# Optimization experiments

Measured on AMD Instinct MI355X. Metric: run time of the kernel, lower is better.

The kernel has to match this reference:

```python
import jax, jax.numpy as jnp
import numpy as np

NUM_CLASSES = 21


def setup_inputs() -> dict:
    key = jax.random.key(0)
    k1, k2 = jax.random.split(key)
    B, C, H, W = 8, NUM_CLASSES, 512, 512
    inputs = jax.random.normal(k1, (B, C, H, W), dtype=jnp.float32)
    targets = jax.random.randint(k2, (B, H, W), 0, C, dtype=jnp.int64)
    return {"inputs": inputs, "targets": targets}


def reference(inputs, targets):
    # inputs: [B, C, H, W] logits; targets: [B, H, W] int labels
    B, C, H, W = inputs.shape
    # Hard predictions are detached in the original (Variable(inputs.data...))
    predicts = jax.lax.stop_gradient(jnp.argmax(inputs, axis=1))  # [B, H, W]
    probs = jax.nn.softmax(inputs, axis=1)                        # [B, C, H, W]

    classes = jnp.arange(C)
    # Per-class binary masks, vectorized over C.
    # Note: the original's i==0 branch (invert nonzero/zero) reduces to the
    # same (x == i) indicator as the i>0 branch.
    pm = predicts[:, None, :, :] == classes[None, :, None, None]  # [B, C, H, W] bool
    tm = targets[:, None, :, :] == classes[None, :, None, None]   # [B, C, H, W] bool
    union_mask = (pm | tm).astype(probs.dtype)      # union with 2 -> 1 clamp
    intersect_mask = (pm & tm).astype(probs.dtype)

    # Soft-weighted per-class sums over batch-flattened spatial dims.
    union = jnp.sum(probs * union_mask, axis=(2, 3))        # [B, C]
    intersect = jnp.sum(probs * intersect_mask, axis=(2, 3))  # [B, C]

    ratio = intersect / jnp.maximum(union, 1.0)  # [B, C]
    # Per class: MSELoss(ratio, 1) = mean over batch; then sum over classes.
    iou_loss = jnp.sum(jnp.mean((ratio - 1.0) ** 2, axis=0))
    return iou_loss
```

## Files before the change

### kernel.cpp

```cpp
#include <hip/hip_runtime.h>

#define NCLS 21
#define HW (512 * 512)
#define BATCH 8
#define GRIDX 128
#define BLOCK 256
#define QUADS_PER_BLOCK ((HW / 4) / GRIDX)
#define ITERS (QUADS_PER_BLOCK / BLOCK)

#define WS_FLOATS (2 * BATCH * NCLS)

__global__ void zero_ws_kernel(float* ws) {
    int i = blockIdx.x * blockDim.x + threadIdx.x;
    if (i < WS_FLOATS) ws[i] = 0.0f;
}

__global__ __launch_bounds__(BLOCK) void iou_partial_kernel(
        const float* __restrict__ in,
        const int* __restrict__ tgt,
        float* __restrict__ ws) {
    const int b = blockIdx.y;
    const float4* __restrict__ in4 = (const float4*)(in + (size_t)b * NCLS * HW);
    const int4*   __restrict__ tb4 = (const int4*)(tgt + (size_t)b * HW);

    float u_acc[NCLS];
    float i_acc[NCLS];
    #pragma unroll
    for (int c = 0; c < NCLS; ++c) { u_acc[c] = 0.0f; i_acc[c] = 0.0f; }

    const int qbase = blockIdx.x * QUADS_PER_BLOCK;

    for (int it = 0; it < ITERS; ++it) {
        const int q = qbase + it * BLOCK + threadIdx.x;
        const int4 tq = tb4[q];
        const int t[4] = {tq.x, tq.y, tq.z, tq.w};

        float m[4], s[4], vt[4];
        int   am[4];

        {
            const float4 x = in4[q];
            const float v[4] = {x.x, x.y, x.z, x.w};
            #pragma unroll
            for (int j = 0; j < 4; ++j) {
                m[j] = v[j]; s[j] = 1.0f; am[j] = 0; vt[j] = v[j];
            }
        }
        #pragma unroll
        for (int c = 1; c < NCLS; ++c) {
            const float4 x = in4[(size_t)c * (HW / 4) + q];
            const float v[4] = {x.x, x.y, x.z, x.w};
            #pragma unroll
            for (int j = 0; j < 4; ++j) {
                const float mn = fmaxf(m[j], v[j]);
                s[j] = s[j] * __expf(m[j] - mn) + __expf(v[j] - mn);
                am[j] = (v[j] > m[j]) ? c : am[j];
                m[j] = mn;
                vt[j] = (c == t[j]) ? v[j] : vt[j];
            }
        }

        #pragma unroll
        for (int j = 0; j < 4; ++j) {
            const float inv    = 1.0f / s[j];
            const float p_pred = inv;
            const float p_t    = __expf(vt[j] - m[j]) * inv;
            const int   tj = t[j], aj = am[j];
            const float w_t = (tj == aj) ? 0.0f : p_t;
            const float ip  = (tj == aj) ? p_pred : 0.0f;
            #pragma unroll
            for (int c = 0; c < NCLS; ++c) {
                u_acc[c] += ((c == aj) ? p_pred : 0.0f) + ((c == tj) ? w_t : 0.0f);
                i_acc[c] += (c == aj) ? ip : 0.0f;
            }
        }
    }

    #pragma unroll
    for (int c = 0; c < NCLS; ++c) {
        #pragma unroll
        for (int off = 32; off > 0; off >>= 1) {
            u_acc[c] += __shfl_down(u_acc[c], off, 64);
            i_acc[c] += __shfl_down(i_acc[c], off, 64);
        }
    }

    __shared__ float s_u[NCLS];
    __shared__ float s_i[NCLS];
    if (threadIdx.x < NCLS) { s_u[threadIdx.x] = 0.0f; s_i[threadIdx.x] = 0.0f; }
    __syncthreads();
    if ((threadIdx.x & 63) == 0) {
        #pragma unroll
        for (int c = 0; c < NCLS; ++c) {
            atomicAdd(&s_u[c], u_acc[c]);
            atomicAdd(&s_i[c], i_acc[c]);
        }
    }
    __syncthreads();
    if (threadIdx.x < NCLS) {
        atomicAdd(&ws[b * NCLS + threadIdx.x], s_u[threadIdx.x]);
        atomicAdd(&ws[BATCH * NCLS + b * NCLS + threadIdx.x], s_i[threadIdx.x]);
    }
}

__global__ __launch_bounds__(BLOCK) void finalize_kernel(
        const float* __restrict__ ws, float* __restrict__ out) {
    __shared__ float red[BLOCK];
    const int i = threadIdx.x;
    float val = 0.0f;
    if (i < BATCH * NCLS) {
        const float u  = ws[i];
        const float it = ws[BATCH * NCLS + i];
        const float ratio = it / fmaxf(u, 1.0f);
        const float d = ratio - 1.0f;
        val = d * d;
    }
    red[i] = val;
    __syncthreads();
    for (int off = BLOCK / 2; off > 0; off >>= 1) {
        if (i < off) red[i] += red[i + off];
        __syncthreads();
    }
    if (i == 0) out[0] = red[0] / (float)BATCH;
}

extern "C" void kernel_launch(void* const* d_in, const int* in_sizes, int n_in,
                              void* d_out, int out_size, void* d_ws, size_t ws_size,
                              hipStream_t stream) {
    const float* in  = (const float*)d_in[0];
    const int*   tgt = (const int*)d_in[1];
    float* ws  = (float*)d_ws;
    float* out = (float*)d_out;

    zero_ws_kernel<<<1, 512, 0, stream>>>(ws);
    dim3 grid(GRIDX, BATCH);
    iou_partial_kernel<<<grid, BLOCK, 0, stream>>>(in, tgt, ws);
    finalize_kernel<<<1, BLOCK, 0, stream>>>(ws, out);
}
```

Measured before the change: 256.5 us.

## Issue all class loads up front, one quad per thread, two-pass softmax

Each thread now handles exactly one quad of pixels. It issues all 21 class float4 loads at once before any compute, which replaces the strided per-block loop and doubles the grid to cover the image. The online softmax is replaced by a max/argmax pass followed by a separate exp-sum pass, which removes the rescaling exp per class. The aim is more memory-level parallelism and fewer exp calls. In exchange, register pressure is high (84 floats of inputs plus 42 accumulators), and the cross-block reduction and atomics now happen twice as often per pixel.

Measured after the change: 256.9 us. No clear change (+0.2%).

```diff
diff --git a/kernel.cpp b/kernel.cpp
--- a/kernel.cpp
+++ b/kernel.cpp
@@ -2,11 +2,10 @@
 
 #define NCLS 21
 #define HW (512 * 512)
+#define NQ (HW / 4)
 #define BATCH 8
-#define GRIDX 128
+#define GRIDX 256
 #define BLOCK 256
-#define QUADS_PER_BLOCK ((HW / 4) / GRIDX)
-#define ITERS (QUADS_PER_BLOCK / BLOCK)
 
 #define WS_FLOATS (2 * BATCH * NCLS)
 
@@ -23,56 +22,53 @@
     const float4* __restrict__ in4 = (const float4*)(in + (size_t)b * NCLS * HW);
     const int4*   __restrict__ tb4 = (const int4*)(tgt + (size_t)b * HW);
 
+    const int q = blockIdx.x * BLOCK + threadIdx.x;
+
+    const int4 tq = tb4[q];
+    float4 x[NCLS];
+    #pragma unroll
+    for (int c = 0; c < NCLS; ++c)
+        x[c] = in4[(size_t)c * NQ + q];
+
+    const int t[4] = {tq.x, tq.y, tq.z, tq.w};
+    float vj[4][NCLS];
+    #pragma unroll
+    for (int c = 0; c < NCLS; ++c) {
+        vj[0][c] = x[c].x; vj[1][c] = x[c].y; vj[2][c] = x[c].z; vj[3][c] = x[c].w;
+    }
+
     float u_acc[NCLS];
     float i_acc[NCLS];
     #pragma unroll
     for (int c = 0; c < NCLS; ++c) { u_acc[c] = 0.0f; i_acc[c] = 0.0f; }
 
-    const int qbase = blockIdx.x * QUADS_PER_BLOCK;
-
-    for (int it = 0; it < ITERS; ++it) {
-        const int q = qbase + it * BLOCK + threadIdx.x;
-        const int4 tq = tb4[q];
-        const int t[4] = {tq.x, tq.y, tq.z, tq.w};
-
-        float m[4], s[4], vt[4];
-        int   am[4];
-
-        {
-            const float4 x = in4[q];
-            const float v[4] = {x.x, x.y, x.z, x.w};
-            #pragma unroll
-            for (int j = 0; j < 4; ++j) {
-                m[j] = v[j]; s[j] = 1.0f; am[j] = 0; vt[j] = v[j];
-            }
-        }
+    #pragma unroll
+    for (int j = 0; j < 4; ++j) {
+        float m = vj[j][0];
+        int   aj = 0;
+        float vt = vj[j][0];
         #pragma unroll
         for (int c = 1; c < NCLS; ++c) {
-            const float4 x = in4[(size_t)c * (HW / 4) + q];
-            const float v[4] = {x.x, x.y, x.z, x.w};
-            #pragma unroll
-            for (int j = 0; j < 4; ++j) {
-                const float mn = fmaxf(m[j], v[j]);
-                s[j] = s[j] * __expf(m[j] - mn) + __expf(v[j] - mn);
-                am[j] = (v[j] > m[j]) ? c : am[j];
-                m[j] = mn;
-                vt[j] = (c == t[j]) ? v[j] : vt[j];
-            }
+            const float v = vj[j][c];
+            aj = (v > m) ? c : aj;
+            m  = fmaxf(m, v);
+            vt = (c == t[j]) ? v : vt;
         }
+        float s = 0.0f;
+        #pragma unroll
+        for (int c = 0; c < NCLS; ++c)
+            s += __expf(vj[j][c] - m);
 
+        const float inv    = 1.0f / s;
+        const float p_pred = inv;
+        const float p_t    = __expf(vt - m) * inv;
+        const int   tj = t[j];
+        const float w_t = (tj == aj) ? 0.0f : p_t;
+        const float ip  = (tj == aj) ? p_pred : 0.0f;
         #pragma unroll
-        for (int j = 0; j < 4; ++j) {
-            const float inv    = 1.0f / s[j];
-            const float p_pred = inv;
-            const float p_t    = __expf(vt[j] - m[j]) * inv;
-            const int   tj = t[j], aj = am[j];
-            const float w_t = (tj == aj) ? 0.0f : p_t;
-            const float ip  = (tj == aj) ? p_pred : 0.0f;
-            #pragma unroll
-            for (int c = 0; c < NCLS; ++c) {
-                u_acc[c] += ((c == aj) ? p_pred : 0.0f) + ((c == tj) ? w_t : 0.0f);
-                i_acc[c] += (c == aj) ? ip : 0.0f;
-            }
+        for (int c = 0; c < NCLS; ++c) {
+            u_acc[c] += ((c == aj) ? p_pred : 0.0f) + ((c == tj) ? w_t : 0.0f);
+            i_acc[c] += (c == aj) ? ip : 0.0f;
         }
     }
 
```
